# Optimization experiments

Measured on AMD Instinct MI355X. Metric: run time of the kernel, lower is better.

The kernel has to match this reference:

```python
import math
import jax, jax.numpy as jnp
import numpy as np

B, IMG, P, D, DEPTH, NH, HD = 8, 384, 16, 768, 12, 12, 64
NREG, NS, NF = 4, 5, 16            # registers, special tokens (1 cls + 4 reg), rope freqs
HP = IMG // P                      # 24 patches per side
NPATCH = HP * HP                   # 576
ROPE_DIM = 2 * NF                  # 32
SCALE = HD ** -0.5


def setup_inputs() -> dict:
    key = jax.random.key(0)
    ks = jax.random.split(key, 12)
    s = 0.02
    rn = lambda k, shape: (jax.random.normal(k, shape, jnp.float32) * s)
    L, DF = DEPTH, 4 * D
    inp = {
        "pixel_values": jax.random.normal(ks[0], (B, 3, IMG, IMG), jnp.float32),
        "conv_w": rn(ks[1], (D, 3, P, P)),
        "conv_b": jnp.zeros((D,), jnp.float32),
        "cls_token": rn(ks[2], (1, 1, D)),
        "storage_tokens": rn(ks[3], (1, NREG, D)),
        "periods": jnp.exp(jnp.linspace(0.0, math.log(100.0), NF)).astype(jnp.float32),
        "ln1_s": jnp.ones((L, D), jnp.float32),
        "ln1_b": jnp.zeros((L, D), jnp.float32),
        "qkv_w": rn(ks[4], (L, 3 * D, D)),
        "qkv_b": rn(ks[5], (L, 3 * D)),
        "bias_mask": jnp.zeros((L, 3 * D), jnp.float32),  # buffer init zeros -> bias nulled
        "proj_w": rn(ks[6], (L, D, D)),
        "proj_b": jnp.zeros((L, D), jnp.float32),
        "ls1": jnp.ones((L, D), jnp.float32),
        "ln2_s": jnp.ones((L, D), jnp.float32),
        "ln2_b": jnp.zeros((L, D), jnp.float32),
        "fc1_w": rn(ks[7], (L, DF, D)),
        "fc1_b": jnp.zeros((L, DF), jnp.float32),
        "fc2_w": rn(ks[8], (L, D, DF)),
        "fc2_b": jnp.zeros((L, D), jnp.float32),
        "ls2": jnp.ones((L, D), jnp.float32),
        "lnf_s": jnp.ones((D,), jnp.float32),
        "lnf_b": jnp.zeros((D,), jnp.float32),
    }
    return inp


def _ln(x, s, b):
    mu = x.mean(-1, keepdims=True)
    var = ((x - mu) ** 2).mean(-1, keepdims=True)
    return (x - mu) / jnp.sqrt(var + 1e-6) * s + b


def _rot(x, cos, sin):
    # x: [b, h, n_patch, 2*NF]; cos/sin: [n_patch, NF]; interleaved even/odd rotation
    even, odd = x[..., 0::2], x[..., 1::2]
    return jnp.stack([even * cos - odd * sin, even * sin + odd * cos], axis=-1).reshape(x.shape)


def _forward(pixel_values, conv_w, conv_b, cls_token, storage_tokens, periods,
             ln1_s, ln1_b, qkv_w, qkv_b, bias_mask, proj_w, proj_b, ls1,
             ln2_s, ln2_b, fc1_w, fc1_b, fc2_w, fc2_b, ls2, lnf_s, lnf_b):
    b = pixel_values.shape[0]
    # Patch embed: stride == kernel conv as reshape + einsum
    xp = pixel_values.reshape(b, 3, HP, P, HP, P)
    tok = jnp.einsum('bchpwq,dcpq->bhwd', xp, conv_w) + conv_b       # [b,HP,HP,D]
    tok = tok.reshape(b, NPATCH, D)
    x = jnp.concatenate([jnp.broadcast_to(cls_token, (b, 1, D)),
                         jnp.broadcast_to(storage_tokens, (b, NREG, D)), tok], axis=1)
    n = x.shape[1]

    # RoPE tables (periods buffer; freqs = 2*pi / periods)
    freqs = (2.0 * math.pi) / periods                                 # [NF]
    pos = jnp.arange(HP, dtype=jnp.float32)
    gy, gx = jnp.meshgrid(pos, pos, indexing='ij')
    ax = gx.reshape(-1, 1) * freqs                                    # [NPATCH, NF]
    ay = gy.reshape(-1, 1) * freqs
    cos_x, sin_x = jnp.cos(ax), jnp.sin(ax)
    cos_y, sin_y = jnp.cos(ay), jnp.sin(ay)

    def blk(h, p):
        (l1s, l1b, qw, qb, bm, pw, pb, g1, l2s, l2b, f1w, f1b, f2w, f2b, g2) = p
        h1 = _ln(h, l1s, l1b)
        qkv = h1 @ qw.T + qb * bm                                     # bias nulled by mask
        qkv = qkv.reshape(b, n, 3, NH, HD).transpose(2, 0, 3, 1, 4)   # [3,b,NH,n,HD]
        q, k, v = qkv[0], qkv[1], qkv[2]
        # rotary on patch tokens; rope_total == HD so the whole head is rotated
        qp, kp = q[:, :, NS:], k[:, :, NS:]
        qp = jnp.concatenate([_rot(qp[..., :ROPE_DIM], cos_x, sin_x),
                              _rot(qp[..., ROPE_DIM:], cos_y, sin_y)], axis=-1)
        kp = jnp.concatenate([_rot(kp[..., :ROPE_DIM], cos_x, sin_x),
                              _rot(kp[..., ROPE_DIM:], cos_y, sin_y)], axis=-1)
        q = jnp.concatenate([q[:, :, :NS], qp], axis=2)
        k = jnp.concatenate([k[:, :, :NS], kp], axis=2)
        attn = jax.nn.softmax(jnp.einsum('bhqd,bhkd->bhqk', q, k) * SCALE, axis=-1)
        o = jnp.einsum('bhqk,bhkd->bhqd', attn, v).transpose(0, 2, 1, 3).reshape(b, n, D)
        h = h + g1 * (o @ pw.T + pb)
        h2 = _ln(h, l2s, l2b)
        m = jax.nn.gelu(h2 @ f1w.T + f1b, approximate=False) @ f2w.T + f2b
        h = h + g2 * m
        return h, None

    params = (ln1_s, ln1_b, qkv_w, qkv_b, bias_mask, proj_w, proj_b, ls1,
              ln2_s, ln2_b, fc1_w, fc1_b, fc2_w, fc2_b, ls2)
    x, _ = jax.lax.scan(blk, x, params)
    return _ln(x, lnf_s, lnf_b)


def reference(pixel_values, conv_w, conv_b, cls_token, storage_tokens, periods,
              ln1_s, ln1_b, qkv_w, qkv_b, bias_mask, proj_w, proj_b, ls1,
              ln2_s, ln2_b, fc1_w, fc1_b, fc2_w, fc2_b, ls2, lnf_s, lnf_b):
    return _forward(pixel_values, conv_w, conv_b, cls_token, storage_tokens, periods,
                    ln1_s, ln1_b, qkv_w, qkv_b, bias_mask, proj_w, proj_b, ls1,
                    ln2_s, ln2_b, fc1_w, fc1_b, fc2_w, fc2_b, ls2, lnf_s, lnf_b)
```

## Files before the change

kernel.cpp:

```cpp
#include <hip/hip_runtime.h>
#include <math.h>

typedef unsigned short u16;
typedef __attribute__((ext_vector_type(8))) short bf8;
typedef __attribute__((ext_vector_type(4))) float f4;

#define DEV static __device__ __forceinline__

DEV u16 f2b(float f){
  unsigned u = __builtin_bit_cast(unsigned, f);
  u += 0x7fffu + ((u >> 16) & 1u);
  return (u16)(u >> 16);
}
DEV float b2f(u16 h){
  unsigned u = ((unsigned)h) << 16;
  return __builtin_bit_cast(float, u);
}

#define BATCH  8
#define NTOK   581
#define NPAD   640
#define DIM    768
#define DFF    3072
#define NHEAD  12
#define HDIM   64
#define NLAYER 12
#define MTOK   (BATCH*NTOK)
#define MPAD2  4736
#define MCONV  (BATCH*576)
#define ATTN_SCALE 0.125f
#define BHEADS (BATCH*NHEAD)
#define QSZ    ((long long)BHEADS*NPAD*HDIM)

enum { EPI_CONV=0, EPI_QKV, EPI_PROJ, EPI_GELU, EPI_FC2 };

DEV int xcdswz(int lin, int n){
  int q = n >> 3, r = n & 7;
  int x = lin & 7, o = lin >> 3;
  return (x < r ? x*(q+1) : r*(q+1) + (x - r)*q) + o;
}

template<int EPI, int BM, int BN>
__global__ __launch_bounds__(256) void gemmRS(
    const u16* __restrict__ A, int lda,
    const u16* __restrict__ B, int ldb, int K,
    const float* __restrict__ bias,
    const float* __restrict__ aux,
    float* __restrict__ Cf,
    u16* __restrict__ Cb)
{
  constexpr int MR = BM / 32, NR = BN / 32;
  constexpr int AL = BM / 64, BL = BN / 64;
  const int gx = gridDim.x;
  const int lin = blockIdx.y * gx + blockIdx.x;
  const int tix = xcdswz(lin, gx * gridDim.y);
  const int bm = (tix / gx) * BM, bn = (tix % gx) * BN;
  __shared__ __attribute__((aligned(16))) u16 As[2][BM][40];
  __shared__ __attribute__((aligned(16))) u16 Bs[2][BN][40];
  const int tid  = threadIdx.x;
  const int lane = tid & 63, wid = tid >> 6;
  const int wr = wid >> 1, wc = wid & 1;
  const int srow = tid >> 2, scol = (tid & 3) * 8;
  const u16* gA[AL]; const u16* gB[BL];
  #pragma unroll
  for (int i = 0; i < AL; ++i) gA[i] = A + (long long)(bm + i*64 + srow) * lda + scol;
  #pragma unroll
  for (int i = 0; i < BL; ++i) gB[i] = B + (long long)(bn + i*64 + srow) * ldb + scol;
  const int frow = lane & 15, quad = lane >> 4, fk = quad * 8;

  f4 acc[MR][NR] = {};
  const int T = K >> 5;

  bf8 xA[AL], xB[BL], yA[AL], yB[BL];
  auto loadX = [&](int kt){
    #pragma unroll
    for (int i = 0; i < AL; ++i) xA[i] = *(const bf8*)(gA[i] + kt*32);
    #pragma unroll
    for (int i = 0; i < BL; ++i) xB[i] = *(const bf8*)(gB[i] + kt*32);
  };
  auto loadY = [&](int kt){
    #pragma unroll
    for (int i = 0; i < AL; ++i) yA[i] = *(const bf8*)(gA[i] + kt*32);
    #pragma unroll
    for (int i = 0; i < BL; ++i) yB[i] = *(const bf8*)(gB[i] + kt*32);
  };
  auto storeX = [&](int buf){
    #pragma unroll
    for (int i = 0; i < AL; ++i) *(bf8*)&As[buf][i*64 + srow][scol] = xA[i];
    #pragma unroll
    for (int i = 0; i < BL; ++i) *(bf8*)&Bs[buf][i*64 + srow][scol] = xB[i];
  };
  auto storeY = [&](int buf){
    #pragma unroll
    for (int i = 0; i < AL; ++i) *(bf8*)&As[buf][i*64 + srow][scol] = yA[i];
    #pragma unroll
    for (int i = 0; i < BL; ++i) *(bf8*)&Bs[buf][i*64 + srow][scol] = yB[i];
  };
  auto compute = [&](int buf){
    bf8 af[MR], bf[NR];
    #pragma unroll
    for (int m = 0; m < MR; ++m)
      af[m] = *(const bf8*)&As[buf][wr*(BM/2) + m*16 + frow][fk];
    #pragma unroll
    for (int n = 0; n < NR; ++n)
      bf[n] = *(const bf8*)&Bs[buf][wc*(BN/2) + n*16 + frow][fk];
    #pragma unroll
    for (int m = 0; m < MR; ++m)
    #pragma unroll
    for (int n = 0; n < NR; ++n)
      acc[m][n] = __builtin_amdgcn_mfma_f32_16x16x32_bf16(af[m], bf[n], acc[m][n], 0, 0, 0);
  };

  loadX(0); loadY(1);
  storeX(0);
  __syncthreads();

  for (int t = 0; t < T; t += 2){
    if (t + 2 < T) loadX(t + 2);
    storeY(1);
    compute(0);
    __syncthreads();
    if (t + 3 < T) loadY(t + 3);
    if (t + 2 < T) storeX(0);
    compute(1);
    __syncthreads();
  }

  #pragma unroll
  for (int mi = 0; mi < MR; ++mi)
  #pragma unroll
  for (int ni = 0; ni < NR; ++ni){
    f4 v = acc[mi][ni];
    int col = bn + wc*(BN/2) + ni*16 + frow;
    int r0  = bm + wr*(BM/2) + mi*16 + quad*4;
    #pragma unroll
    for (int j = 0; j < 4; ++j){
      int m = r0 + j;
      float val = v[j];
      if constexpr (EPI == EPI_CONV){
        int b = m / 576, p = m % 576;
        Cf[((long long)b*NTOK + 5 + p)*DIM + col] = val + bias[col];
      } else if constexpr (EPI == EPI_QKV){
        if (m < MTOK){
          int b = m / NTOK, tt = m % NTOK;
          int which = col / DIM, rem = col % DIM;
          int h = rem / HDIM, hd = rem % HDIM;
          float x = val + bias[col];
          if (which == 0) x *= ATTN_SCALE;
          if (which < 2 && tt >= 5){
            float po = __shfl_xor(x, 1);
            int p = tt - 5;
            int f = (hd & 31) >> 1;
            int pc = (hd < 32) ? (p % 24) : (p / 24);
            float c = aux[pc*16 + f];
            float s = aux[384 + pc*16 + f];
            x = (hd & 1) ? (po*s + x*c) : (x*c - po*s);
          }
          long long bh = (long long)(b*NHEAD + h);
          if (which == 2)
            Cb[2*QSZ + (bh*HDIM + hd)*NPAD + tt] = f2b(x);
          else
            Cb[(long long)which*QSZ + (bh*NPAD + tt)*HDIM + hd] = f2b(x);
        }
      } else if constexpr (EPI == EPI_PROJ || EPI == EPI_FC2){
        if (m < MTOK)
          Cf[(long long)m*DIM + col] += aux[col] * (val + bias[col]);
      } else if constexpr (EPI == EPI_GELU){
        float x = val + bias[col];
        float g = 0.5f * x * (1.0f + erff(x * 0.70710678118f));
        Cb[(long long)m*DFF + col] = f2b(g);
      }
    }
  }
}

__global__ __launch_bounds__(256) void flash_k(
    const u16* __restrict__ Q, const u16* __restrict__ K,
    const u16* __restrict__ VT, u16* __restrict__ obuf)
{
  const int lid = blockIdx.x;
  const int xcd = lid & 7, slot = lid >> 3;
  const int bh = xcd * 12 + slot / 5;
  const int qb = slot % 5;
  const int b = bh / NHEAD, h = bh % NHEAD;
  const int tid = threadIdx.x, lane = tid & 63, w = tid >> 6;
  const int frow = lane & 15, quad = lane >> 4;
  __shared__ u16 P[4][2][16][80];
  const u16* Qb = Q  + (long long)bh * NPAD * HDIM;
  const u16* Kb = K  + (long long)bh * NPAD * HDIM;
  const u16* Vb = VT + (long long)bh * HDIM * NPAD;
  bf8 qa0[2], qa1[2];
  #pragma unroll
  for (int bd = 0; bd < 2; ++bd){
    const u16* qr = &Qb[(qb*128 + bd*64 + w*16 + frow)*HDIM + quad*8];
    qa0[bd] = *(const bf8*)qr;
    qa1[bd] = *(const bf8*)(qr + 32);
  }
  f4 o[2][4] = {};
  float m[2][4], l[2][4];
  #pragma unroll
  for (int bd = 0; bd < 2; ++bd)
  #pragma unroll
  for (int j = 0; j < 4; ++j){ m[bd][j] = -1e30f; l[bd][j] = 0.0f; }

  bf8 kb0[4], kb1[4];
  #pragma unroll
  for (int n = 0; n < 4; ++n){
    const u16* kr = &Kb[(n*16 + frow)*HDIM + quad*8];
    kb0[n] = *(const bf8*)kr;
    kb1[n] = *(const bf8*)(kr + 32);
  }

  for (int kt = 0; kt < NPAD/64; ++kt){
    bf8 vb0[4], vb1[4];
    #pragma unroll
    for (int n = 0; n < 4; ++n){
      const u16* vr = &Vb[(n*16 + frow)*NPAD + kt*64 + quad*8];
      vb0[n] = *(const bf8*)vr;
      vb1[n] = *(const bf8*)(vr + 32);
    }
    f4 s[2][4];
    #pragma unroll
    for (int n = 0; n < 4; ++n)
    #pragma unroll
    for (int bd = 0; bd < 2; ++bd){
      f4 z = {};
      z        = __builtin_amdgcn_mfma_f32_16x16x32_bf16(qa0[bd], kb0[n], z, 0, 0, 0);
      s[bd][n] = __builtin_amdgcn_mfma_f32_16x16x32_bf16(qa1[bd], kb1[n], z, 0, 0, 0);
    }
    if (kt + 1 < NPAD/64){
      #pragma unroll
      for (int n = 0; n < 4; ++n){
        const u16* kr = &Kb[((kt+1)*64 + n*16 + frow)*HDIM + quad*8];
        kb0[n] = *(const bf8*)kr;
        kb1[n] = *(const bf8*)(kr + 32);
      }
    }
    if (kt == NPAD/64 - 1){
      #pragma unroll
      for (int n = 0; n < 4; ++n){
        int kcol = kt*64 + n*16 + frow;
        if (kcol >= NTOK){
          #pragma unroll
          for (int bd = 0; bd < 2; ++bd)
            s[bd][n][0] = s[bd][n][1] = s[bd][n][2] = s[bd][n][3] = -1e30f;
        }
      }
    }
    #pragma unroll
    for (int bd = 0; bd < 2; ++bd){
      float sc[4];
      #pragma unroll
      for (int j = 0; j < 4; ++j){
        float v = fmaxf(fmaxf(s[bd][0][j], s[bd][1][j]), fmaxf(s[bd][2][j], s[bd][3][j]));
        v = fmaxf(v, __shfl_xor(v, 1));  v = fmaxf(v, __shfl_xor(v, 2));
        v = fmaxf(v, __shfl_xor(v, 4));  v = fmaxf(v, __shfl_xor(v, 8));
        float mn = fmaxf(m[bd][j], v);
        sc[j] = __expf(m[bd][j] - mn);
        m[bd][j] = mn;
      }
      float ts[4] = {0.f, 0.f, 0.f, 0.f};
      #pragma unroll
      for (int n = 0; n < 4; ++n){
        #pragma unroll
        for (int j = 0; j < 4; ++j){
          float p = __expf(s[bd][n][j] - m[bd][j]);
          ts[j] += p;
          P[w][bd][quad*4 + j][n*16 + frow] = f2b(p);
        }
      }
      #pragma unroll
      for (int j = 0; j < 4; ++j){
        float v = ts[j];
        v += __shfl_xor(v, 1); v += __shfl_xor(v, 2);
        v += __shfl_xor(v, 4); v += __shfl_xor(v, 8);
        l[bd][j] = l[bd][j]*sc[j] + v;
      }
      #pragma unroll
      for (int n = 0; n < 4; ++n)
      #pragma unroll
      for (int j = 0; j < 4; ++j) o[bd][n][j] *= sc[j];
      bf8 pa0 = *(const bf8*)&P[w][bd][frow][quad*8];
      bf8 pa1 = *(const bf8*)&P[w][bd][frow][quad*8 + 32];
      #pragma unroll
      for (int n = 0; n < 4; ++n){
        o[bd][n] = __builtin_amdgcn_mfma_f32_16x16x32_bf16(pa0, vb0[n], o[bd][n], 0, 0, 0);
        o[bd][n] = __builtin_amdgcn_mfma_f32_16x16x32_bf16(pa1, vb1[n], o[bd][n], 0, 0, 0);
      }
    }
  }
  #pragma unroll
  for (int bd = 0; bd < 2; ++bd)
  #pragma unroll
  for (int j = 0; j < 4; ++j){
    int t = qb*128 + bd*64 + w*16 + quad*4 + j;
    if (t < NTOK){
      float inv = 1.0f / l[bd][j];
      #pragma unroll
      for (int n = 0; n < 4; ++n)
        obuf[((long long)b*NTOK + t)*DIM + h*HDIM + n*16 + frow] = f2b(o[bd][n][j] * inv);
    }
  }
}

template<int F32OUT>
__global__ __launch_bounds__(256) void ln_k(const float* __restrict__ x,
    const float* __restrict__ s, const float* __restrict__ b,
    u16* __restrict__ ob, float* __restrict__ of)
{
  const long long row = blockIdx.x;
  const float* xr = x + row * DIM;
  const int t = threadIdx.x;
  float v0 = xr[t], v1 = xr[t + 256], v2 = xr[t + 512];
  float sum = v0 + v1 + v2;
  #pragma unroll
  for (int o = 32; o; o >>= 1) sum += __shfl_down(sum, o);
  __shared__ float r1[4], r2[4];
  const int lane = t & 63, w = t >> 6;
  if (lane == 0) r1[w] = sum;
  __syncthreads();
  float mu = (r1[0] + r1[1] + r1[2] + r1[3]) * (1.0f / DIM);
  float d0 = v0 - mu, d1 = v1 - mu, d2 = v2 - mu;
  float vs = d0*d0 + d1*d1 + d2*d2;
  #pragma unroll
  for (int o = 32; o; o >>= 1) vs += __shfl_down(vs, o);
  if (lane == 0) r2[w] = vs;
  __syncthreads();
  float inv = 1.0f / sqrtf((r2[0] + r2[1] + r2[2] + r2[3]) * (1.0f / DIM) + 1e-6f);
  if constexpr (F32OUT){
    float* orow = of + row * DIM;
    orow[t]       = d0 * inv * s[t]       + b[t];
    orow[t + 256] = d1 * inv * s[t + 256] + b[t + 256];
    orow[t + 512] = d2 * inv * s[t + 512] + b[t + 512];
  } else {
    u16* orow = ob + row * DIM;
    orow[t]       = f2b(d0 * inv * s[t]       + b[t]);
    orow[t + 256] = f2b(d1 * inv * s[t + 256] + b[t + 256]);
    orow[t + 512] = f2b(d2 * inv * s[t + 512] + b[t + 512]);
  }
}

__global__ void ropetab_k(const float* __restrict__ periods, float* __restrict__ tab)
{
  int idx = blockIdx.x * blockDim.x + threadIdx.x;
  if (idx >= 24 * 16) return;
  int c = idx >> 4, f = idx & 15;
  float fr = 6.283185307179586f / periods[f];
  float a = (float)c * fr;
  tab[idx]       = cosf(a);
  tab[384 + idx] = sinf(a);
}

__global__ void initx_k(float* __restrict__ x, const float* __restrict__ cls,
                        const float* __restrict__ stor)
{
  int idx = blockIdx.x * blockDim.x + threadIdx.x;
  if (idx >= BATCH * 5 * DIM) return;
  int d = idx % DIM; int t = (idx / DIM) % 5; int b = idx / (5 * DIM);
  x[((long long)b * NTOK + t) * DIM + d] = (t == 0) ? cls[d] : stor[(t - 1) * DIM + d];
}

__global__ void patch_k(const float* __restrict__ px, u16* __restrict__ Ap)
{
  int idx = blockIdx.x * blockDim.x + threadIdx.x;
  if (idx >= MCONV * DIM) return;
  int k = idx % DIM, m = idx / DIM;
  int b = m / 576, r = m % 576, hp = r / 24, wp = r % 24;
  int c = k / 256, rem = k % 256, p = rem / 16, q = rem % 16;
  float v = px[((((long long)b * 3 + c) * 384) + hp * 16 + p) * 384 + wp * 16 + q];
  Ap[idx] = f2b(v);
}

__global__ void cvt_k(const float* __restrict__ src, u16* __restrict__ dst, long long n)
{
  long long i = (long long)blockIdx.x * blockDim.x + threadIdx.x;
  long long stride = (long long)gridDim.x * blockDim.x;
  for (; i < n; i += stride) dst[i] = f2b(src[i]);
}

__global__ void biaseff_k(const float* __restrict__ qb, const float* __restrict__ bm,
                          float* __restrict__ out, int n)
{
  int i = blockIdx.x * blockDim.x + threadIdx.x;
  if (i < n) out[i] = qb[i] * bm[i];
}

extern "C" void kernel_launch(void* const* d_in, const int* in_sizes, int n_in,
                              void* d_out, int out_size, void* d_ws, size_t ws_size,
                              hipStream_t stream)
{
  const float* pixel   = (const float*)d_in[0];
  const float* conv_w  = (const float*)d_in[1];
  const float* conv_b  = (const float*)d_in[2];
  const float* cls     = (const float*)d_in[3];
  const float* stor    = (const float*)d_in[4];
  const float* periods = (const float*)d_in[5];
  const float* ln1s    = (const float*)d_in[6];
  const float* ln1b    = (const float*)d_in[7];
  const float* qkvw    = (const float*)d_in[8];
  const float* qkvb    = (const float*)d_in[9];
  const float* bmask   = (const float*)d_in[10];
  const float* projw   = (const float*)d_in[11];
  const float* projb   = (const float*)d_in[12];
  const float* ls1     = (const float*)d_in[13];
  const float* ln2s    = (const float*)d_in[14];
  const float* ln2b    = (const float*)d_in[15];
  const float* fc1w    = (const float*)d_in[16];
  const float* fc1b    = (const float*)d_in[17];
  const float* fc2w    = (const float*)d_in[18];
  const float* fc2b    = (const float*)d_in[19];
  const float* ls2     = (const float*)d_in[20];
  const float* lnfs    = (const float*)d_in[21];
  const float* lnfb    = (const float*)d_in[22];

  char* wsp = (char*)d_ws;
  auto alloc = [&](long long bytes) -> char* {
    char* p = wsp; wsp += (bytes + 255) & ~255LL; return p;
  };
  u16*   wqkv  = (u16*)  alloc((long long)NLAYER*2304*768*2);
  u16*   wproj = (u16*)  alloc((long long)NLAYER*768*768*2);
  u16*   wfc1  = (u16*)  alloc((long long)NLAYER*3072*768*2);
  u16*   wfc2  = (u16*)  alloc((long long)NLAYER*768*3072*2);
  u16*   wconv = (u16*)  alloc((long long)768*768*2);
  float* beff  = (float*)alloc((long long)NLAYER*2304*4);
  float* x     = (float*)alloc((long long)MPAD2*DIM*4);
  u16*   h     = (u16*)  alloc((long long)MPAD2*DIM*2);
  u16*   obuf  = (u16*)  alloc((long long)MPAD2*DIM*2);
  u16*   mlp   = (u16*)  alloc((long long)MPAD2*DFF*2);
  u16*   Ap    = (u16*)  alloc((long long)MCONV*DIM*2);
  u16*   Q     = (u16*)  alloc(QSZ*2*3);
  u16*   Kb    = Q + QSZ;
  u16*   VT    = Q + 2*QSZ;
  float* tab   = (float*)alloc((long long)2*24*16*4);
  if ((size_t)(wsp - (char*)d_ws) > ws_size) return;

  auto cvt = [&](const float* src, u16* dst, long long n){
    long long nb = (n + 255) / 256; if (nb > 4096) nb = 4096;
    cvt_k<<<(int)nb, 256, 0, stream>>>(src, dst, n);
  };
  cvt(qkvw,  wqkv,  (long long)NLAYER*2304*768);
  cvt(projw, wproj, (long long)NLAYER*768*768);
  cvt(fc1w,  wfc1,  (long long)NLAYER*3072*768);
  cvt(fc2w,  wfc2,  (long long)NLAYER*768*3072);
  cvt(conv_w, wconv, (long long)768*768);
  biaseff_k<<<(NLAYER*2304 + 255)/256, 256, 0, stream>>>(qkvb, bmask, beff, NLAYER*2304);
  ropetab_k<<<2, 256, 0, stream>>>(periods, tab);
  hipMemsetAsync(Q, 0, (size_t)QSZ*2*3, stream);

  patch_k<<<(MCONV*DIM + 255)/256, 256, 0, stream>>>(pixel, Ap);
  initx_k<<<(BATCH*5*DIM + 255)/256, 256, 0, stream>>>(x, cls, stor);
  gemmRS<EPI_CONV,64,128><<<dim3(DIM/128, MCONV/64), 256, 0, stream>>>(
      Ap, DIM, wconv, DIM, DIM, conv_b, nullptr, x, nullptr);

  for (int l = 0; l < NLAYER; ++l){
    ln_k<0><<<MTOK, 256, 0, stream>>>(x, ln1s + l*DIM, ln1b + l*DIM, h, nullptr);
    gemmRS<EPI_QKV,128,128><<<dim3(2304/128, MPAD2/128), 256, 0, stream>>>(
        h, DIM, wqkv + (long long)l*2304*768, DIM, DIM,
        beff + l*2304, tab, nullptr, Q);
    flash_k<<<dim3(480), 256, 0, stream>>>(Q, Kb, VT, obuf);
    gemmRS<EPI_PROJ,64,128><<<dim3(DIM/128, MPAD2/64), 256, 0, stream>>>(
        obuf, DIM, wproj + (long long)l*768*768, DIM, DIM,
        projb + l*DIM, ls1 + l*DIM, x, nullptr);
    ln_k<0><<<MTOK, 256, 0, stream>>>(x, ln2s + l*DIM, ln2b + l*DIM, h, nullptr);
    gemmRS<EPI_GELU,128,128><<<dim3(DFF/128, MPAD2/128), 256, 0, stream>>>(
        h, DIM, wfc1 + (long long)l*3072*768, DIM, DIM,
        fc1b + l*DFF, nullptr, nullptr, mlp);
    gemmRS<EPI_FC2,64,128><<<dim3(DIM/128, MPAD2/64), 256, 0, stream>>>(
        mlp, DFF, wfc2 + (long long)l*768*3072, DFF, DFF,
        fc2b + l*DIM, ls2 + l*DIM, x, nullptr);
  }
  ln_k<1><<<MTOK, 256, 0, stream>>>(x, lnfs, lnfb, nullptr, (float*)d_out);
}
```

Before: 3.491 ms.

## Retune GEMM wave counts and tiles; add lazy rescaling and priority hints to attention

The GEMM kernel gains a wave-count template parameter. QKV and FC1 now run with 8 waves (512 threads) on 128x128 tiles, while conv, proj and FC2 use 64x64 tiles with 4 waves, giving more blocks on the narrow-N GEMMs. In flash attention, the running-max rescale of o and l is skipped unless some row's max grows by more than 8, which removes exp and multiply work on most tiles. MFMA sections are also wrapped in s_setprio hints. Lazy rescaling lets unnormalized probabilities reach up to e^8 before bf16 conversion, which is a small precision risk.

After: 3.115 ms. 1.12x faster.

```diff
diff --git a/kernel.cpp b/kernel.cpp
--- a/kernel.cpp
+++ b/kernel.cpp
@@ -40,8 +40,8 @@
   return (x < r ? x*(q+1) : r*(q+1) + (x - r)*q) + o;
 }
 
-template<int EPI, int BM, int BN>
-__global__ __launch_bounds__(256) void gemmRS(
+template<int EPI, int BM, int BN, int NWAVE>
+__global__ __launch_bounds__(NWAVE*64) void gemmRS(
     const u16* __restrict__ A, int lda,
     const u16* __restrict__ B, int ldb, int K,
     const float* __restrict__ bias,
@@ -49,8 +49,13 @@
     float* __restrict__ Cf,
     u16* __restrict__ Cb)
 {
-  constexpr int MR = BM / 32, NR = BN / 32;
-  constexpr int AL = BM / 64, BL = BN / 64;
+  constexpr int NT = NWAVE * 64;
+  constexpr int SR = NT / 4;
+  constexpr int AL = BM / SR, BL = BN / SR;
+  constexpr int WROWS = (NWAVE == 8) ? 4 : 2;
+  constexpr int WCOLS = NWAVE / WROWS;
+  constexpr int TR = BM / WROWS, TC = BN / WCOLS;
+  constexpr int MR = TR / 16, NR = TC / 16;
   const int gx = gridDim.x;
   const int lin = blockIdx.y * gx + blockIdx.x;
   const int tix = xcdswz(lin, gx * gridDim.y);
@@ -59,13 +64,13 @@
   __shared__ __attribute__((aligned(16))) u16 Bs[2][BN][40];
   const int tid  = threadIdx.x;
   const int lane = tid & 63, wid = tid >> 6;
-  const int wr = wid >> 1, wc = wid & 1;
+  const int wr = wid % WROWS, wc = wid / WROWS;
   const int srow = tid >> 2, scol = (tid & 3) * 8;
   const u16* gA[AL]; const u16* gB[BL];
   #pragma unroll
-  for (int i = 0; i < AL; ++i) gA[i] = A + (long long)(bm + i*64 + srow) * lda + scol;
-  #pragma unroll
-  for (int i = 0; i < BL; ++i) gB[i] = B + (long long)(bn + i*64 + srow) * ldb + scol;
+  for (int i = 0; i < AL; ++i) gA[i] = A + (long long)(bm + i*SR + srow) * lda + scol;
+  #pragma unroll
+  for (int i = 0; i < BL; ++i) gB[i] = B + (long long)(bn + i*SR + srow) * ldb + scol;
   const int frow = lane & 15, quad = lane >> 4, fk = quad * 8;
 
   f4 acc[MR][NR] = {};
@@ -86,24 +91,24 @@
   };
   auto storeX = [&](int buf){
     #pragma unroll
-    for (int i = 0; i < AL; ++i) *(bf8*)&As[buf][i*64 + srow][scol] = xA[i];
-    #pragma unroll
-    for (int i = 0; i < BL; ++i) *(bf8*)&Bs[buf][i*64 + srow][scol] = xB[i];
+    for (int i = 0; i < AL; ++i) *(bf8*)&As[buf][i*SR + srow][scol] = xA[i];
+    #pragma unroll
+    for (int i = 0; i < BL; ++i) *(bf8*)&Bs[buf][i*SR + srow][scol] = xB[i];
   };
   auto storeY = [&](int buf){
     #pragma unroll
-    for (int i = 0; i < AL; ++i) *(bf8*)&As[buf][i*64 + srow][scol] = yA[i];
-    #pragma unroll
-    for (int i = 0; i < BL; ++i) *(bf8*)&Bs[buf][i*64 + srow][scol] = yB[i];
+    for (int i = 0; i < AL; ++i) *(bf8*)&As[buf][i*SR + srow][scol] = yA[i];
+    #pragma unroll
+    for (int i = 0; i < BL; ++i) *(bf8*)&Bs[buf][i*SR + srow][scol] = yB[i];
   };
   auto compute = [&](int buf){
     bf8 af[MR], bf[NR];
     #pragma unroll
     for (int m = 0; m < MR; ++m)
-      af[m] = *(const bf8*)&As[buf][wr*(BM/2) + m*16 + frow][fk];
+      af[m] = *(const bf8*)&As[buf][wr*TR + m*16 + frow][fk];
     #pragma unroll
     for (int n = 0; n < NR; ++n)
-      bf[n] = *(const bf8*)&Bs[buf][wc*(BN/2) + n*16 + frow][fk];
+      bf[n] = *(const bf8*)&Bs[buf][wc*TC + n*16 + frow][fk];
     #pragma unroll
     for (int m = 0; m < MR; ++m)
     #pragma unroll
@@ -131,8 +136,8 @@
   #pragma unroll
   for (int ni = 0; ni < NR; ++ni){
     f4 v = acc[mi][ni];
-    int col = bn + wc*(BN/2) + ni*16 + frow;
-    int r0  = bm + wr*(BM/2) + mi*16 + quad*4;
+    int col = bn + wc*TC + ni*16 + frow;
+    int r0  = bm + wr*TR + mi*16 + quad*4;
     #pragma unroll
     for (int j = 0; j < 4; ++j){
       int m = r0 + j;
@@ -220,6 +225,7 @@
       vb1[n] = *(const bf8*)(vr + 32);
     }
     f4 s[2][4];
+    __builtin_amdgcn_s_setprio(1);
     #pragma unroll
     for (int n = 0; n < 4; ++n)
     #pragma unroll
@@ -228,6 +234,7 @@
       z        = __builtin_amdgcn_mfma_f32_16x16x32_bf16(qa0[bd], kb0[n], z, 0, 0, 0);
       s[bd][n] = __builtin_amdgcn_mfma_f32_16x16x32_bf16(qa1[bd], kb1[n], z, 0, 0, 0);
     }
+    __builtin_amdgcn_s_setprio(0);
     if (kt + 1 < NPAD/64){
       #pragma unroll
       for (int n = 0; n < 4; ++n){
@@ -249,15 +256,26 @@
     }
     #pragma unroll
     for (int bd = 0; bd < 2; ++bd){
-      float sc[4];
+      float tv[4];
+      int need = 0;
       #pragma unroll
       for (int j = 0; j < 4; ++j){
         float v = fmaxf(fmaxf(s[bd][0][j], s[bd][1][j]), fmaxf(s[bd][2][j], s[bd][3][j]));
         v = fmaxf(v, __shfl_xor(v, 1));  v = fmaxf(v, __shfl_xor(v, 2));
         v = fmaxf(v, __shfl_xor(v, 4));  v = fmaxf(v, __shfl_xor(v, 8));
-        float mn = fmaxf(m[bd][j], v);
-        sc[j] = __expf(m[bd][j] - mn);
-        m[bd][j] = mn;
+        tv[j] = v;
+        need |= (v > m[bd][j] + 8.0f) ? 1 : 0;
+      }
+      if (__any(need)){
+        #pragma unroll
+        for (int j = 0; j < 4; ++j){
+          float mn = fmaxf(m[bd][j], tv[j]);
+          float sc = __expf(m[bd][j] - mn);
+          m[bd][j] = mn;
+          l[bd][j] *= sc;
+          #pragma unroll
+          for (int n = 0; n < 4; ++n) o[bd][n][j] *= sc;
+        }
       }
       float ts[4] = {0.f, 0.f, 0.f, 0.f};
       #pragma unroll
@@ -274,19 +292,17 @@
         float v = ts[j];
         v += __shfl_xor(v, 1); v += __shfl_xor(v, 2);
         v += __shfl_xor(v, 4); v += __shfl_xor(v, 8);
-        l[bd][j] = l[bd][j]*sc[j] + v;
-      }
-      #pragma unroll
-      for (int n = 0; n < 4; ++n)
-      #pragma unroll
-      for (int j = 0; j < 4; ++j) o[bd][n][j] *= sc[j];
+        l[bd][j] += v;
+      }
       bf8 pa0 = *(const bf8*)&P[w][bd][frow][quad*8];
       bf8 pa1 = *(const bf8*)&P[w][bd][frow][quad*8 + 32];
+      __builtin_amdgcn_s_setprio(1);
       #pragma unroll
       for (int n = 0; n < 4; ++n){
         o[bd][n] = __builtin_amdgcn_mfma_f32_16x16x32_bf16(pa0, vb0[n], o[bd][n], 0, 0, 0);
         o[bd][n] = __builtin_amdgcn_mfma_f32_16x16x32_bf16(pa1, vb1[n], o[bd][n], 0, 0, 0);
       }
+      __builtin_amdgcn_s_setprio(0);
     }
   }
   #pragma unroll
@@ -449,23 +465,23 @@
 
   patch_k<<<(MCONV*DIM + 255)/256, 256, 0, stream>>>(pixel, Ap);
   initx_k<<<(BATCH*5*DIM + 255)/256, 256, 0, stream>>>(x, cls, stor);
-  gemmRS<EPI_CONV,64,128><<<dim3(DIM/128, MCONV/64), 256, 0, stream>>>(
+  gemmRS<EPI_CONV,64,64,4><<<dim3(DIM/64, MCONV/64), 256, 0, stream>>>(
       Ap, DIM, wconv, DIM, DIM, conv_b, nullptr, x, nullptr);
 
   for (int l = 0; l < NLAYER; ++l){
     ln_k<0><<<MTOK, 256, 0, stream>>>(x, ln1s + l*DIM, ln1b + l*DIM, h, nullptr);
-    gemmRS<EPI_QKV,128,128><<<dim3(2304/128, MPAD2/128), 256, 0, stream>>>(
+    gemmRS<EPI_QKV,128,128,8><<<dim3(2304/128, MPAD2/128), 512, 0, stream>>>(
         h, DIM, wqkv + (long long)l*2304*768, DIM, DIM,
         beff + l*2304, tab, nullptr, Q);
     flash_k<<<dim3(480), 256, 0, stream>>>(Q, Kb, VT, obuf);
-    gemmRS<EPI_PROJ,64,128><<<dim3(DIM/128, MPAD2/64), 256, 0, stream>>>(
+    gemmRS<EPI_PROJ,64,64,4><<<dim3(DIM/64, MPAD2/64), 256, 0, stream>>>(
         obuf, DIM, wproj + (long long)l*768*768, DIM, DIM,
         projb + l*DIM, ls1 + l*DIM, x, nullptr);
     ln_k<0><<<MTOK, 256, 0, stream>>>(x, ln2s + l*DIM, ln2b + l*DIM, h, nullptr);
-    gemmRS<EPI_GELU,128,128><<<dim3(DFF/128, MPAD2/128), 256, 0, stream>>>(
+    gemmRS<EPI_GELU,128,128,8><<<dim3(DFF/128, MPAD2/128), 512, 0, stream>>>(
         h, DIM, wfc1 + (long long)l*3072*768, DIM, DIM,
         fc1b + l*DFF, nullptr, nullptr, mlp);
-    gemmRS<EPI_FC2,64,128><<<dim3(DIM/128, MPAD2/64), 256, 0, stream>>>(
+    gemmRS<EPI_FC2,64,64,4><<<dim3(DIM/64, MPAD2/64), 256, 0, stream>>>(
         mlp, DFF, wfc2 + (long long)l*768*3072, DFF, DFF,
         fc2b + l*DIM, ls2 + l*DIM, x, nullptr);
   }
```
